# Kernel tuning notes

Measured on AMD Instinct MI355X. Metric: run time of the kernel, lower is better.

Reference implementation:

```python
import jax, jax.numpy as jnp
import numpy as np

H = 16  # number of heads

def setup_inputs() -> dict:
    key = jax.random.key(0)
    ks = jax.random.split(key, 8)
    B, T, D = 4, 2048, 1024
    s = 0.02
    return {
        "query": jax.random.normal(ks[0], (B, T, D), jnp.float32),
        "key":   jax.random.normal(ks[1], (B, T, D), jnp.float32),
        "value": jax.random.normal(ks[2], (B, T, D), jnp.float32),
        "mask":  jnp.ones((B, T, T), jnp.int32),
        # torch nn.Linear weights: [out_features, in_features]
        "Wq": jax.random.normal(ks[3], (D, D), jnp.float32) * s,
        "Wk": jax.random.normal(ks[4], (D, D), jnp.float32) * s,
        "Wv": jax.random.normal(ks[5], (D, D), jnp.float32) * s,
        "Wo": jax.random.normal(ks[6], (D, D), jnp.float32) * s,
        "bo": jnp.zeros((D,), jnp.float32),
    }

def reference(query, key, value, mask, Wq, Wk, Wv, Wo, bo):
    B, Tq, _ = query.shape
    Tk = key.shape[1]
    Dv = Wv.shape[0]
    # linear projections (y = x @ W^T), split into heads: [B, H, T, dh]
    Q = jnp.einsum('btd,ed->bte', query, Wq).reshape(B, Tq, H, -1).transpose(0, 2, 1, 3)
    K = jnp.einsum('btd,ed->bte', key,   Wk).reshape(B, Tk, H, -1).transpose(0, 2, 1, 3)
    V = jnp.einsum('btd,ed->bte', value, Wv).reshape(B, Tk, H, -1).transpose(0, 2, 1, 3)
    d_k = K.shape[-1]
    scores = jnp.einsum('bhqd,bhkd->bhqk', Q, K) / jnp.sqrt(jnp.asarray(d_k, Q.dtype))
    # mask broadcast: [B,1,Tq,Tk]; masked_fill(mask==0, -1e9)
    scores = jnp.where(mask[:, None] == 0, jnp.asarray(-1e9, scores.dtype), scores)
    attn = jax.nn.softmax(scores, axis=-1)
    Z = jnp.einsum('bhqk,bhkd->bhqd', attn, V)          # [B,H,Tq,dh]
    Zc = Z.transpose(0, 2, 1, 3).reshape(B, Tq, Dv)     # concat heads
    return jnp.einsum('btd,ed->bte', Zc, Wo) + bo
```

## Files before the change

kernel.cpp:

```cpp
#include <hip/hip_runtime.h>

typedef __bf16 bf16x8 __attribute__((ext_vector_type(8)));
typedef __bf16 bf16x4 __attribute__((ext_vector_type(4)));
typedef float f32x4 __attribute__((ext_vector_type(4)));
typedef unsigned short u16;
typedef unsigned long long u64;

#define NX 8388608
#define NW 1048576

__device__ __forceinline__ u16 f2bf(float f) {
  union { float f; unsigned u; } c; c.f = f;
  unsigned u = c.u;
  u += 0x7fffu + ((u >> 16) & 1u);
  return (u16)(u >> 16);
}

__device__ __forceinline__ f32x4 mfma16(bf16x8 a, bf16x8 b, f32x4 c) {
  return __builtin_amdgcn_mfma_f32_16x16x32_bf16(a, b, c, 0, 0, 0);
}

__device__ __forceinline__ void gld16(void* lds, const void* g) {
  __builtin_amdgcn_global_load_lds(
      (const __attribute__((address_space(1))) unsigned int*)g,
      (__attribute__((address_space(3))) unsigned int*)lds, 16, 0, 0);
}

__global__ __launch_bounds__(256) void cast_all(
    const float* __restrict__ q, const float* __restrict__ k,
    const float* __restrict__ v, const float* __restrict__ wq,
    const float* __restrict__ wk, const float* __restrict__ wv,
    const float* __restrict__ wo, u16* __restrict__ xbf, u16* __restrict__ wbf) {
  long long i = ((long long)blockIdx.x * 256 + threadIdx.x) * 8;
  const float* src; u16* dst; long long off;
  if (i < (long long)NX)            { src = q; dst = xbf;            off = i; }
  else if (i < 2LL * NX)            { src = k; dst = xbf + NX;       off = i - NX; }
  else if (i < 3LL * NX)            { src = v; dst = xbf + 2LL * NX; off = i - 2LL * NX; }
  else {
    long long j = i - 3LL * NX;
    int w = (int)(j / NW); off = j - (long long)w * NW;
    src = (w == 0) ? wq : (w == 1) ? wk : (w == 2) ? wv : wo;
    dst = wbf + (long long)w * NW;
  }
  float4 a = *(const float4*)(src + off);
  float4 b = *(const float4*)(src + off + 4);
  u16 o[8] = {f2bf(a.x), f2bf(a.y), f2bf(a.z), f2bf(a.w),
              f2bf(b.x), f2bf(b.y), f2bf(b.z), f2bf(b.w)};
  *(uint4*)(dst + off) = *(const uint4*)o;
}

__global__ __launch_bounds__(256) void mask_pack(
    const int* __restrict__ mask, u64* __restrict__ bits) {
  const int row = blockIdx.x * 4 + (threadIdx.x >> 6);
  const int lane = threadIdx.x & 63;
  const int* mrow = mask + (long long)row * 2048;
#pragma unroll
  for (int it = 0; it < 32; it++) {
    u64 w = __ballot(mrow[it * 64 + lane] != 0);
    if (lane == 0) bits[row * 32 + it] = w;
  }
}

template <int MODE>
__global__ __launch_bounds__(256, 2) void gemm128(
    const u16* __restrict__ Abase, const u16* __restrict__ Wbase,
    u16* __restrict__ oq, u16* __restrict__ ok, u16* __restrict__ ovt,
    const float* __restrict__ bias, float* __restrict__ of) {
  __shared__ u16 smem[2][128 * 64];
  u16* sA = smem[0];
  u16* sB = smem[1];
  const u16* A = Abase;
  const u16* W = Wbase;
  if (MODE == 0) { A += (long long)blockIdx.z * NX; W += (long long)blockIdx.z * NW; }
  const int tid = threadIdx.x, wave = tid >> 6, lane = tid & 63;
  const int quad = lane >> 4, l15 = lane & 15;
  const int m0 = blockIdx.y * 128, n0 = blockIdx.x * 128;
  const int wm = (wave & 1) * 64, wn = (wave >> 1) * 64;
  const int lr = lane >> 3;
  const int gc = (lane & 7) ^ lr;
  f32x4 acc[4][4];
#pragma unroll
  for (int i = 0; i < 4; i++)
#pragma unroll
    for (int j = 0; j < 4; j++) acc[i][j] = (f32x4){0.f, 0.f, 0.f, 0.f};

  for (int ks = 0; ks < 16; ks++) {
    const int k0 = ks * 64;
    __syncthreads();
#pragma unroll
    for (int t = 0; t < 4; t++) {
      const int rb = wave * 32 + t * 8;
      gld16(&sA[rb * 64], &A[(m0 + rb + lr) * 1024 + k0 + gc * 8]);
      gld16(&sB[rb * 64], &W[(n0 + rb + lr) * 1024 + k0 + gc * 8]);
    }
    __syncthreads();
#pragma unroll
    for (int kc = 0; kc < 2; kc++) {
      bf16x8 aF[4], bF[4];
#pragma unroll
      for (int i = 0; i < 4; i++)
        aF[i] = *(const bf16x8*)&sA[(wm + 16 * i + l15) * 64 +
                                    (((kc * 4 + quad) ^ (l15 & 7)) * 8)];
#pragma unroll
      for (int j = 0; j < 4; j++)
        bF[j] = *(const bf16x8*)&sB[(wn + 16 * j + l15) * 64 +
                                    (((kc * 4 + quad) ^ (l15 & 7)) * 8)];
#pragma unroll
      for (int i = 0; i < 4; i++)
#pragma unroll
        for (int j = 0; j < 4; j++) acc[i][j] = mfma16(aF[i], bF[j], acc[i][j]);
    }
  }

  if (MODE == 0) {
    const int z = blockIdx.z;
    if (z < 2) {
      const float qscale = (z == 0) ? 0.18033688f : 1.0f;
      u16* dst = (z == 0) ? oq : ok;
#pragma unroll
      for (int i = 0; i < 4; i++)
#pragma unroll
        for (int j = 0; j < 4; j++)
#pragma unroll
          for (int r = 0; r < 4; r++) {
            int m = m0 + wm + 16 * i + quad * 4 + r;
            int n = n0 + wn + 16 * j + l15;
            int b = m >> 11, t = m & 2047, h = n >> 6, d = n & 63;
            dst[(((b << 4) + h) * 2048 + t) * 64 + d] = f2bf(acc[i][j][r] * qscale);
          }
    } else {
      __syncthreads();
      u16* sT = &smem[0][0] + wave * 4096;
#pragma unroll
      for (int i = 0; i < 4; i++)
#pragma unroll
        for (int j = 0; j < 4; j++)
#pragma unroll
          for (int r = 0; r < 4; r++) {
            int m = 16 * i + quad * 4 + r;
            int n = 16 * j + l15;
            sT[n * 64 + (((m >> 3) ^ (n & 7)) * 8) + (m & 7)] = f2bf(acc[i][j][r]);
          }
      const int b = m0 >> 11, t0 = (m0 + wm) & 2047;
      const int h = (n0 + wn) >> 6;
      u16* dst = ovt + ((long long)((b << 4) + h)) * 131072 + lane * 2048 + t0;
#pragma unroll
      for (int c = 0; c < 8; c++) {
        uint4 val = *(const uint4*)&sT[lane * 64 + ((c ^ (lane & 7)) * 8)];
        *(uint4*)(dst + c * 8) = val;
      }
    }
  } else {
    float bb[4];
#pragma unroll
    for (int j = 0; j < 4; j++) bb[j] = bias[n0 + wn + 16 * j + l15];
#pragma unroll
    for (int i = 0; i < 4; i++)
#pragma unroll
      for (int j = 0; j < 4; j++)
#pragma unroll
        for (int r = 0; r < 4; r++) {
          int m = m0 + wm + 16 * i + quad * 4 + r;
          int n = n0 + wn + 16 * j + l15;
          of[m * 1024 + n] = acc[i][j][r] + bb[j];
        }
  }
}

__device__ __forceinline__ void stage_tile(
    u16* sKb, u16* sVb, const u16* __restrict__ Kh, const u16* __restrict__ Vt,
    int bh, int kt, int wave, int lr8, int gc8) {
#pragma unroll
  for (int t = 0; t < 2; t++) {
    const int rb = wave * 16 + t * 8;
    const int c = rb + lr8;
    const int kap = ((c & 15) << 2) + (c >> 4);
    gld16(&sKb[rb * 64], &Kh[(bh * 2048 + kt * 64 + kap) * 64 + gc8 * 8]);
    gld16(&sVb[rb * 64], &Vt[(bh * 64 + rb + lr8) * 2048 + kt * 64 + gc8 * 8]);
  }
}

__global__ __launch_bounds__(256, 3) void attn(
    const u16* __restrict__ Qh, const u16* __restrict__ Kh,
    const u16* __restrict__ Vt, const u64* __restrict__ mbits,
    u16* __restrict__ Zc) {
  __shared__ u16 sK[2][64 * 64];
  __shared__ u16 sV[2][64 * 64];
  __shared__ alignas(16) u16 sP[4][32][72];
  const int tid = threadIdx.x, wave = tid >> 6, lane = tid & 63;
  const int quad = lane >> 4, l15 = lane & 15;
  const int id = blockIdx.y * 16 + blockIdx.x;
  const int id2 = (id & 7) * 128 + (id >> 3);
  const int bh = id2 >> 4, qt = id2 & 15;
  const int b = bh >> 4, h = bh & 15;
  const int q0 = qt * 128 + wave * 32;
  const int lr8 = lane >> 3, gc8 = (lane & 7) ^ lr8;

  bf16x8 qa[2][2];
#pragma unroll
  for (int g = 0; g < 2; g++)
#pragma unroll
    for (int kc = 0; kc < 2; kc++)
      qa[g][kc] = *(const bf16x8*)&Qh[(bh * 2048 + q0 + g * 16 + l15) * 64 +
                                      kc * 32 + quad * 8];

  const u64* mrow = mbits + (long long)(b * 2048 + q0) * 32;
  u64 am = ~0ull;
#pragma unroll
  for (int i = 0; i < 16; i++) am &= mrow[lane * 16 + i];
  const bool allfull = __all(am == ~0ull);

  const u64* mb[2];
#pragma unroll
  for (int g = 0; g < 2; g++)
    mb[g] = mbits + (long long)(b * 2048 + q0 + g * 16 + quad * 4) * 32;

  f32x4 oacc[2][4];
#pragma unroll
  for (int g = 0; g < 2; g++)
#pragma unroll
    for (int j = 0; j < 4; j++) oacc[g][j] = (f32x4){0.f, 0.f, 0.f, 0.f};
  float lv[2][4] = {{0.f, 0.f, 0.f, 0.f}, {0.f, 0.f, 0.f, 0.f}};

  stage_tile(&sK[0][0], &sV[0][0], Kh, Vt, bh, 0, wave, lr8, gc8);

  for (int kt = 0; kt < 32; kt++) {
    const int cur = kt & 1;
    __syncthreads();

    u64 mw[2][4];
    if (!allfull) {
#pragma unroll
      for (int g = 0; g < 2; g++)
#pragma unroll
        for (int r = 0; r < 4; r++) mw[g][r] = mb[g][r * 32 + kt];
    }
    if (kt < 31)
      stage_tile(&sK[cur ^ 1][0], &sV[cur ^ 1][0], Kh, Vt, bh, kt + 1,
                 wave, lr8, gc8);

    f32x4 sacc[2][4];
#pragma unroll
    for (int g = 0; g < 2; g++)
#pragma unroll
      for (int j = 0; j < 4; j++) sacc[g][j] = (f32x4){0.f, 0.f, 0.f, 0.f};
#pragma unroll
    for (int kc = 0; kc < 2; kc++)
#pragma unroll
      for (int j = 0; j < 4; j++) {
        bf16x8 kF = *(const bf16x8*)&sK[cur][(16 * j + l15) * 64 +
                                            (((kc * 4 + quad) ^ (l15 & 7)) * 8)];
        sacc[0][j] = mfma16(qa[0][kc], kF, sacc[0][j]);
        sacc[1][j] = mfma16(qa[1][kc], kF, sacc[1][j]);
      }

    if (allfull) {
#pragma unroll
      for (int g = 0; g < 2; g++)
#pragma unroll
        for (int r = 0; r < 4; r++) {
          bf16x4 pk;
          float ls = 0.f;
#pragma unroll
          for (int j = 0; j < 4; j++) {
            float p = __builtin_amdgcn_exp2f(sacc[g][j][r]);
            ls += p;
            pk[j] = (__bf16)p;
          }
          lv[g][r] += ls;
          *(bf16x4*)&sP[wave][g * 16 + quad * 4 + r][l15 * 4] = pk;
        }
    } else {
#pragma unroll
      for (int g = 0; g < 2; g++)
#pragma unroll
        for (int r = 0; r < 4; r++) {
          bf16x4 pk;
          float ls = 0.f;
          u64 w = mw[g][r];
#pragma unroll
          for (int j = 0; j < 4; j++) {
            float p = __builtin_amdgcn_exp2f(sacc[g][j][r]);
            p = ((w >> (l15 * 4 + j)) & 1ull) ? p : 0.f;
            ls += p;
            pk[j] = (__bf16)p;
          }
          lv[g][r] += ls;
          *(bf16x4*)&sP[wave][g * 16 + quad * 4 + r][l15 * 4] = pk;
        }
    }

#pragma unroll
    for (int kc = 0; kc < 2; kc++) {
      bf16x8 aP0 = *(const bf16x8*)&sP[wave][l15][kc * 32 + quad * 8];
      bf16x8 aP1 = *(const bf16x8*)&sP[wave][16 + l15][kc * 32 + quad * 8];
#pragma unroll
      for (int j = 0; j < 4; j++) {
        bf16x8 vF = *(const bf16x8*)&sV[cur][(16 * j + l15) * 64 +
                                            (((kc * 4 + quad) ^ (l15 & 7)) * 8)];
        oacc[0][j] = mfma16(aP0, vF, oacc[0][j]);
        oacc[1][j] = mfma16(aP1, vF, oacc[1][j]);
      }
    }
  }

#pragma unroll
  for (int g = 0; g < 2; g++) {
    float inv[4];
#pragma unroll
    for (int r = 0; r < 4; r++) {
      float s = lv[g][r];
      s += __shfl_xor(s, 1);
      s += __shfl_xor(s, 2);
      s += __shfl_xor(s, 4);
      s += __shfl_xor(s, 8);
      inv[r] = 1.f / s;
    }
#pragma unroll
    for (int j = 0; j < 4; j++)
#pragma unroll
      for (int r = 0; r < 4; r++) {
        int t = q0 + g * 16 + quad * 4 + r;
        Zc[(b * 2048 + t) * 1024 + h * 64 + 16 * j + l15] =
            f2bf(oacc[g][j][r] * inv[r]);
      }
  }
}

extern "C" void kernel_launch(void* const* d_in, const int* in_sizes, int n_in,
                              void* d_out, int out_size, void* d_ws, size_t ws_size,
                              hipStream_t stream) {
  (void)in_sizes; (void)n_in; (void)out_size; (void)ws_size;
  const float* q    = (const float*)d_in[0];
  const float* k    = (const float*)d_in[1];
  const float* v    = (const float*)d_in[2];
  const int*   mask = (const int*)d_in[3];
  const float* Wq   = (const float*)d_in[4];
  const float* Wk   = (const float*)d_in[5];
  const float* Wv   = (const float*)d_in[6];
  const float* Wo   = (const float*)d_in[7];
  const float* bo   = (const float*)d_in[8];
  float* out = (float*)d_out;

  u16* Xbf = (u16*)d_ws;
  u16* Wbf = Xbf + 3LL * NX;
  u16* Qh  = Wbf + 4LL * NW;
  u16* Kh  = Qh + (long long)NX;
  u16* Vt  = Kh + (long long)NX;
  u16* Zc  = Vt + (long long)NX;
  u64* Mb  = (u64*)(Zc + (long long)NX);

  cast_all<<<14336, 256, 0, stream>>>(q, k, v, Wq, Wk, Wv, Wo, Xbf, Wbf);
  mask_pack<<<2048, 256, 0, stream>>>(mask, Mb);
  gemm128<0><<<dim3(8, 64, 3), 256, 0, stream>>>(Xbf, Wbf, Qh, Kh, Vt, nullptr, nullptr);
  attn<<<dim3(16, 64), 256, 0, stream>>>(Qh, Kh, Vt, Mb, Zc);
  gemm128<1><<<dim3(8, 64), 256, 0, stream>>>(Zc, Wbf + 3LL * NW, nullptr, nullptr, nullptr,
                                              bo, out);
}
```

Before: 390.5 us.

## Double per-wave query rows in attention to reuse K/V fragments across more MFMAs

The attention kernel now gives each wave 64 query rows instead of 32, so each block covers 256 queries and the grid is halved. Each K/V fragment read from LDS is reused across four query groups rather than two, and the P buffer uses an XOR-swizzled 64-wide layout so its writes and reads avoid bank conflicts. It also adds s_setprio around the MFMA bursts and reads mask words directly in the loop. In exchange, register pressure rises (launch bounds drop from 3 to 2 blocks per CU) and there are fewer blocks to spread across the CUs.

```diff
diff --git a/kernel.cpp b/kernel.cpp
--- a/kernel.cpp
+++ b/kernel.cpp
@@ -180,25 +180,25 @@
   }
 }
 
-__global__ __launch_bounds__(256, 3) void attn(
+__global__ __launch_bounds__(256, 2) void attn(
     const u16* __restrict__ Qh, const u16* __restrict__ Kh,
     const u16* __restrict__ Vt, const u64* __restrict__ mbits,
     u16* __restrict__ Zc) {
   __shared__ u16 sK[2][64 * 64];
   __shared__ u16 sV[2][64 * 64];
-  __shared__ alignas(16) u16 sP[4][32][72];
+  __shared__ u16 sP[4][64 * 64];
   const int tid = threadIdx.x, wave = tid >> 6, lane = tid & 63;
   const int quad = lane >> 4, l15 = lane & 15;
-  const int id = blockIdx.y * 16 + blockIdx.x;
-  const int id2 = (id & 7) * 128 + (id >> 3);
-  const int bh = id2 >> 4, qt = id2 & 15;
+  const int id = blockIdx.y * 8 + blockIdx.x;
+  const int id2 = (id & 7) * 64 + (id >> 3);
+  const int bh = id2 >> 3, qt = id2 & 7;
   const int b = bh >> 4, h = bh & 15;
-  const int q0 = qt * 128 + wave * 32;
+  const int q0 = qt * 256 + wave * 64;
   const int lr8 = lane >> 3, gc8 = (lane & 7) ^ lr8;
 
-  bf16x8 qa[2][2];
-#pragma unroll
-  for (int g = 0; g < 2; g++)
+  bf16x8 qa[4][2];
+#pragma unroll
+  for (int g = 0; g < 4; g++)
 #pragma unroll
     for (int kc = 0; kc < 2; kc++)
       qa[g][kc] = *(const bf16x8*)&Qh[(bh * 2048 + q0 + g * 16 + l15) * 64 +
@@ -207,56 +207,58 @@
   const u64* mrow = mbits + (long long)(b * 2048 + q0) * 32;
   u64 am = ~0ull;
 #pragma unroll
-  for (int i = 0; i < 16; i++) am &= mrow[lane * 16 + i];
+  for (int i = 0; i < 32; i++) am &= mrow[lane * 32 + i];
   const bool allfull = __all(am == ~0ull);
 
-  const u64* mb[2];
-#pragma unroll
-  for (int g = 0; g < 2; g++)
+  const u64* mb[4];
+#pragma unroll
+  for (int g = 0; g < 4; g++)
     mb[g] = mbits + (long long)(b * 2048 + q0 + g * 16 + quad * 4) * 32;
 
-  f32x4 oacc[2][4];
-#pragma unroll
-  for (int g = 0; g < 2; g++)
+  f32x4 oacc[4][4];
+#pragma unroll
+  for (int g = 0; g < 4; g++)
 #pragma unroll
     for (int j = 0; j < 4; j++) oacc[g][j] = (f32x4){0.f, 0.f, 0.f, 0.f};
-  float lv[2][4] = {{0.f, 0.f, 0.f, 0.f}, {0.f, 0.f, 0.f, 0.f}};
+  float lv[4][4];
+#pragma unroll
+  for (int g = 0; g < 4; g++)
+#pragma unroll
+    for (int r = 0; r < 4; r++) lv[g][r] = 0.f;
 
   stage_tile(&sK[0][0], &sV[0][0], Kh, Vt, bh, 0, wave, lr8, gc8);
+  const f32x4 z4 = (f32x4){0.f, 0.f, 0.f, 0.f};
 
   for (int kt = 0; kt < 32; kt++) {
     const int cur = kt & 1;
     __syncthreads();
-
-    u64 mw[2][4];
-    if (!allfull) {
-#pragma unroll
-      for (int g = 0; g < 2; g++)
-#pragma unroll
-        for (int r = 0; r < 4; r++) mw[g][r] = mb[g][r * 32 + kt];
-    }
     if (kt < 31)
       stage_tile(&sK[cur ^ 1][0], &sV[cur ^ 1][0], Kh, Vt, bh, kt + 1,
                  wave, lr8, gc8);
 
-    f32x4 sacc[2][4];
-#pragma unroll
-    for (int g = 0; g < 2; g++)
-#pragma unroll
-      for (int j = 0; j < 4; j++) sacc[g][j] = (f32x4){0.f, 0.f, 0.f, 0.f};
+    bf16x8 kF[2][4];
 #pragma unroll
     for (int kc = 0; kc < 2; kc++)
 #pragma unroll
-      for (int j = 0; j < 4; j++) {
-        bf16x8 kF = *(const bf16x8*)&sK[cur][(16 * j + l15) * 64 +
+      for (int j = 0; j < 4; j++)
+        kF[kc][j] = *(const bf16x8*)&sK[cur][(16 * j + l15) * 64 +
                                             (((kc * 4 + quad) ^ (l15 & 7)) * 8)];
-        sacc[0][j] = mfma16(qa[0][kc], kF, sacc[0][j]);
-        sacc[1][j] = mfma16(qa[1][kc], kF, sacc[1][j]);
-      }
+    f32x4 sacc[4][4];
+    __builtin_amdgcn_s_setprio(1);
+#pragma unroll
+    for (int j = 0; j < 4; j++)
+#pragma unroll
+      for (int g = 0; g < 4; g++) sacc[g][j] = mfma16(qa[g][0], kF[0][j], z4);
+#pragma unroll
+    for (int j = 0; j < 4; j++)
+#pragma unroll
+      for (int g = 0; g < 4; g++)
+        sacc[g][j] = mfma16(qa[g][1], kF[1][j], sacc[g][j]);
+    __builtin_amdgcn_s_setprio(0);
 
     if (allfull) {
 #pragma unroll
-      for (int g = 0; g < 2; g++)
+      for (int g = 0; g < 4; g++)
 #pragma unroll
         for (int r = 0; r < 4; r++) {
           bf16x4 pk;
@@ -268,16 +270,18 @@
             pk[j] = (__bf16)p;
           }
           lv[g][r] += ls;
-          *(bf16x4*)&sP[wave][g * 16 + quad * 4 + r][l15 * 4] = pk;
+          const int row = g * 16 + quad * 4 + r;
+          *(bf16x4*)&sP[wave][row * 64 + (((l15 >> 1) ^ (row & 7)) * 8) +
+                              (l15 & 1) * 4] = pk;
         }
     } else {
 #pragma unroll
-      for (int g = 0; g < 2; g++)
+      for (int g = 0; g < 4; g++)
 #pragma unroll
         for (int r = 0; r < 4; r++) {
           bf16x4 pk;
           float ls = 0.f;
-          u64 w = mw[g][r];
+          u64 w = mb[g][r * 32 + kt];
 #pragma unroll
           for (int j = 0; j < 4; j++) {
             float p = __builtin_amdgcn_exp2f(sacc[g][j][r]);
@@ -286,26 +290,34 @@
             pk[j] = (__bf16)p;
           }
           lv[g][r] += ls;
-          *(bf16x4*)&sP[wave][g * 16 + quad * 4 + r][l15 * 4] = pk;
+          const int row = g * 16 + quad * 4 + r;
+          *(bf16x4*)&sP[wave][row * 64 + (((l15 >> 1) ^ (row & 7)) * 8) +
+                              (l15 & 1) * 4] = pk;
         }
     }
 
-#pragma unroll
-    for (int kc = 0; kc < 2; kc++) {
-      bf16x8 aP0 = *(const bf16x8*)&sP[wave][l15][kc * 32 + quad * 8];
-      bf16x8 aP1 = *(const bf16x8*)&sP[wave][16 + l15][kc * 32 + quad * 8];
-#pragma unroll
-      for (int j = 0; j < 4; j++) {
-        bf16x8 vF = *(const bf16x8*)&sV[cur][(16 * j + l15) * 64 +
-                                            (((kc * 4 + quad) ^ (l15 & 7)) * 8)];
-        oacc[0][j] = mfma16(aP0, vF, oacc[0][j]);
-        oacc[1][j] = mfma16(aP1, vF, oacc[1][j]);
+    bf16x8 vF[2][4];
+#pragma unroll
+    for (int kc = 0; kc < 2; kc++)
+#pragma unroll
+      for (int j = 0; j < 4; j++)
+        vF[kc][j] = *(const bf16x8*)&sV[cur][(16 * j + l15) * 64 +
+                                             (((kc * 4 + quad) ^ (l15 & 7)) * 8)];
+    __builtin_amdgcn_s_setprio(1);
+#pragma unroll
+    for (int kc = 0; kc < 2; kc++)
+#pragma unroll
+      for (int g = 0; g < 4; g++) {
+        bf16x8 aP = *(const bf16x8*)&sP[wave][(g * 16 + l15) * 64 +
+                                              (((kc * 4 + quad) ^ (l15 & 7)) * 8)];
+#pragma unroll
+        for (int j = 0; j < 4; j++) oacc[g][j] = mfma16(aP, vF[kc][j], oacc[g][j]);
       }
-    }
-  }
-
-#pragma unroll
-  for (int g = 0; g < 2; g++) {
+    __builtin_amdgcn_s_setprio(0);
+  }
+
+#pragma unroll
+  for (int g = 0; g < 4; g++) {
     float inv[4];
 #pragma unroll
     for (int r = 0; r < 4; r++) {
@@ -353,7 +365,7 @@
   cast_all<<<14336, 256, 0, stream>>>(q, k, v, Wq, Wk, Wv, Wo, Xbf, Wbf);
   mask_pack<<<2048, 256, 0, stream>>>(mask, Mb);
   gemm128<0><<<dim3(8, 64, 3), 256, 0, stream>>>(Xbf, Wbf, Qh, Kh, Vt, nullptr, nullptr);
-  attn<<<dim3(16, 64), 256, 0, stream>>>(Qh, Kh, Vt, Mb, Zc);
+  attn<<<dim3(8, 64), 256, 0, stream>>>(Qh, Kh, Vt, Mb, Zc);
   gemm128<1><<<dim3(8, 64), 256, 0, stream>>>(Zc, Wbf + 3LL * NW, nullptr, nullptr, nullptr,
                                               bo, out);
 }
```

After: 393.4 us. About the same (+0.8%).

## Compute transposed scores so P stays in registers, removing LDS round-trip

Applied to the files above, without the earlier changes.

Swaps the MFMA operand order to compute S^T (K as A, Q as B), so each lane's score outputs already line up with the A-operand layout of the PV MFMA. This removes the per-wave sP shared-memory buffer and its writes and reads. The K row permutation is changed to match the new layout, and the row-sum reduction becomes a cross-quad shuffle. It also adds s_setprio around the MFMA blocks and raises launch bounds to 4 blocks/CU, which risks register pressure from preloading all K and V fragments.

```diff
diff --git a/kernel.cpp b/kernel.cpp
--- a/kernel.cpp
+++ b/kernel.cpp
@@ -174,19 +174,18 @@
   for (int t = 0; t < 2; t++) {
     const int rb = wave * 16 + t * 8;
     const int c = rb + lr8;
-    const int kap = ((c & 15) << 2) + (c >> 4);
+    const int kap = (c & 32) + (((c >> 2) & 3) << 3) + ((c & 16) >> 2) + (c & 3);
     gld16(&sKb[rb * 64], &Kh[(bh * 2048 + kt * 64 + kap) * 64 + gc8 * 8]);
     gld16(&sVb[rb * 64], &Vt[(bh * 64 + rb + lr8) * 2048 + kt * 64 + gc8 * 8]);
   }
 }
 
-__global__ __launch_bounds__(256, 3) void attn(
+__global__ __launch_bounds__(256, 4) void attn(
     const u16* __restrict__ Qh, const u16* __restrict__ Kh,
     const u16* __restrict__ Vt, const u64* __restrict__ mbits,
     u16* __restrict__ Zc) {
   __shared__ u16 sK[2][64 * 64];
   __shared__ u16 sV[2][64 * 64];
-  __shared__ alignas(16) u16 sP[4][32][72];
   const int tid = threadIdx.x, wave = tid >> 6, lane = tid & 63;
   const int quad = lane >> 4, l15 = lane & 15;
   const int id = blockIdx.y * 16 + blockIdx.x;
@@ -210,112 +209,109 @@
   for (int i = 0; i < 16; i++) am &= mrow[lane * 16 + i];
   const bool allfull = __all(am == ~0ull);
 
-  const u64* mb[2];
+  f32x4 oacc[2][4];
 #pragma unroll
   for (int g = 0; g < 2; g++)
-    mb[g] = mbits + (long long)(b * 2048 + q0 + g * 16 + quad * 4) * 32;
-
-  f32x4 oacc[2][4];
-#pragma unroll
-  for (int g = 0; g < 2; g++)
 #pragma unroll
     for (int j = 0; j < 4; j++) oacc[g][j] = (f32x4){0.f, 0.f, 0.f, 0.f};
-  float lv[2][4] = {{0.f, 0.f, 0.f, 0.f}, {0.f, 0.f, 0.f, 0.f}};
+  float lv[2] = {0.f, 0.f};
 
   stage_tile(&sK[0][0], &sV[0][0], Kh, Vt, bh, 0, wave, lr8, gc8);
+  const f32x4 z4 = (f32x4){0.f, 0.f, 0.f, 0.f};
 
   for (int kt = 0; kt < 32; kt++) {
     const int cur = kt & 1;
     __syncthreads();
-
-    u64 mw[2][4];
-    if (!allfull) {
-#pragma unroll
-      for (int g = 0; g < 2; g++)
-#pragma unroll
-        for (int r = 0; r < 4; r++) mw[g][r] = mb[g][r * 32 + kt];
-    }
     if (kt < 31)
       stage_tile(&sK[cur ^ 1][0], &sV[cur ^ 1][0], Kh, Vt, bh, kt + 1,
                  wave, lr8, gc8);
 
+    bf16x8 kF[2][4];
+#pragma unroll
+    for (int kc = 0; kc < 2; kc++)
+#pragma unroll
+      for (int j = 0; j < 4; j++)
+        kF[kc][j] = *(const bf16x8*)&sK[cur][(16 * j + l15) * 64 +
+                                            (((kc * 4 + quad) ^ (l15 & 7)) * 8)];
     f32x4 sacc[2][4];
-#pragma unroll
-    for (int g = 0; g < 2; g++)
-#pragma unroll
-      for (int j = 0; j < 4; j++) sacc[g][j] = (f32x4){0.f, 0.f, 0.f, 0.f};
-#pragma unroll
-    for (int kc = 0; kc < 2; kc++)
-#pragma unroll
-      for (int j = 0; j < 4; j++) {
-        bf16x8 kF = *(const bf16x8*)&sK[cur][(16 * j + l15) * 64 +
-                                            (((kc * 4 + quad) ^ (l15 & 7)) * 8)];
-        sacc[0][j] = mfma16(qa[0][kc], kF, sacc[0][j]);
-        sacc[1][j] = mfma16(qa[1][kc], kF, sacc[1][j]);
+    __builtin_amdgcn_s_setprio(1);
+#pragma unroll
+    for (int j = 0; j < 4; j++)
+#pragma unroll
+      for (int g = 0; g < 2; g++) sacc[g][j] = mfma16(kF[0][j], qa[g][0], z4);
+#pragma unroll
+    for (int j = 0; j < 4; j++)
+#pragma unroll
+      for (int g = 0; g < 2; g++)
+        sacc[g][j] = mfma16(kF[1][j], qa[g][1], sacc[g][j]);
+    __builtin_amdgcn_s_setprio(0);
+
+    bf16x8 pa[2][2];
+    if (allfull) {
+#pragma unroll
+      for (int g = 0; g < 2; g++) {
+        float ls = 0.f;
+#pragma unroll
+        for (int kc = 0; kc < 2; kc++) {
+          bf16x8 pk;
+#pragma unroll
+          for (int e = 0; e < 8; e++) {
+            float p = __builtin_amdgcn_exp2f(sacc[g][2 * kc + (e >> 2)][e & 3]);
+            ls += p;
+            pk[e] = (__bf16)p;
+          }
+          pa[g][kc] = pk;
+        }
+        lv[g] += ls;
       }
-
-    if (allfull) {
-#pragma unroll
-      for (int g = 0; g < 2; g++)
-#pragma unroll
-        for (int r = 0; r < 4; r++) {
-          bf16x4 pk;
-          float ls = 0.f;
-#pragma unroll
-          for (int j = 0; j < 4; j++) {
-            float p = __builtin_amdgcn_exp2f(sacc[g][j][r]);
+    } else {
+#pragma unroll
+      for (int g = 0; g < 2; g++) {
+        u64 w = mbits[(long long)(b * 2048 + q0 + g * 16 + l15) * 32 + kt];
+        float ls = 0.f;
+#pragma unroll
+        for (int kc = 0; kc < 2; kc++) {
+          bf16x8 pk;
+#pragma unroll
+          for (int e = 0; e < 8; e++) {
+            float p = __builtin_amdgcn_exp2f(sacc[g][2 * kc + (e >> 2)][e & 3]);
+            p = ((w >> (32 * kc + 8 * quad + e)) & 1ull) ? p : 0.f;
             ls += p;
-            pk[j] = (__bf16)p;
+            pk[e] = (__bf16)p;
           }
-          lv[g][r] += ls;
-          *(bf16x4*)&sP[wave][g * 16 + quad * 4 + r][l15 * 4] = pk;
+          pa[g][kc] = pk;
         }
-    } else {
-#pragma unroll
-      for (int g = 0; g < 2; g++)
-#pragma unroll
-        for (int r = 0; r < 4; r++) {
-          bf16x4 pk;
-          float ls = 0.f;
-          u64 w = mw[g][r];
-#pragma unroll
-          for (int j = 0; j < 4; j++) {
-            float p = __builtin_amdgcn_exp2f(sacc[g][j][r]);
-            p = ((w >> (l15 * 4 + j)) & 1ull) ? p : 0.f;
-            ls += p;
-            pk[j] = (__bf16)p;
-          }
-          lv[g][r] += ls;
-          *(bf16x4*)&sP[wave][g * 16 + quad * 4 + r][l15 * 4] = pk;
-        }
-    }
-
-#pragma unroll
-    for (int kc = 0; kc < 2; kc++) {
-      bf16x8 aP0 = *(const bf16x8*)&sP[wave][l15][kc * 32 + quad * 8];
-      bf16x8 aP1 = *(const bf16x8*)&sP[wave][16 + l15][kc * 32 + quad * 8];
-#pragma unroll
-      for (int j = 0; j < 4; j++) {
-        bf16x8 vF = *(const bf16x8*)&sV[cur][(16 * j + l15) * 64 +
-                                            (((kc * 4 + quad) ^ (l15 & 7)) * 8)];
-        oacc[0][j] = mfma16(aP0, vF, oacc[0][j]);
-        oacc[1][j] = mfma16(aP1, vF, oacc[1][j]);
+        lv[g] += ls;
       }
     }
+
+    bf16x8 vF[2][4];
+#pragma unroll
+    for (int kc = 0; kc < 2; kc++)
+#pragma unroll
+      for (int j = 0; j < 4; j++)
+        vF[kc][j] = *(const bf16x8*)&sV[cur][(16 * j + l15) * 64 +
+                                             (((kc * 4 + quad) ^ (l15 & 7)) * 8)];
+    __builtin_amdgcn_s_setprio(1);
+#pragma unroll
+    for (int kc = 0; kc < 2; kc++)
+#pragma unroll
+      for (int g = 0; g < 2; g++)
+#pragma unroll
+        for (int j = 0; j < 4; j++)
+          oacc[g][j] = mfma16(pa[g][kc], vF[kc][j], oacc[g][j]);
+    __builtin_amdgcn_s_setprio(0);
   }
 
 #pragma unroll
   for (int g = 0; g < 2; g++) {
+    float s = lv[g];
+    s += __shfl_xor(s, 16);
+    s += __shfl_xor(s, 32);
     float inv[4];
 #pragma unroll
-    for (int r = 0; r < 4; r++) {
-      float s = lv[g][r];
-      s += __shfl_xor(s, 1);
-      s += __shfl_xor(s, 2);
-      s += __shfl_xor(s, 4);
-      s += __shfl_xor(s, 8);
-      inv[r] = 1.f / s;
-    }
+    for (int r = 0; r < 4; r++)
+      inv[r] = 1.f / __shfl(s, quad * 4 + r);
 #pragma unroll
     for (int j = 0; j < 4; j++)
 #pragma unroll
```

Result: no change. 392.5 us (+0.5%).
